# Performance work log

Measured on AMD Instinct MI355X. Metric: run time of the kernel, lower is better.

Reference implementation:

```python
import jax, jax.numpy as jnp
import numpy as np


def setup_inputs() -> dict:
    key = jax.random.key(0)
    kq, kk, kv = jax.random.split(key, 3)
    shape = (4, 8, 64, 8192)  # (b, n_heads, d, s)
    q = jax.random.normal(kq, shape, dtype=jnp.float32)
    k = jax.random.normal(kk, shape, dtype=jnp.float32)
    v = jax.random.normal(kv, shape, dtype=jnp.float32)
    return {"q": q, "k": k, "v": v}


def reference(q, k, v):
    # q, k, v: (b, n, d, s)
    q = jax.nn.softmax(q, axis=-2)        # softmax over feature dim d
    k = jax.nn.softmax(k, axis=-1)        # softmax over sequence dim s
    scale = q.shape[-2] ** (-0.5)
    q = q * scale
    # context: (b, n, d_k, d_v) = sum_s k[..., i, s] * v[..., j, s]
    context = jnp.einsum('bnis,bnjs->bnij', k, v)
    # out: (b, n, d_v, s)
    out = jnp.einsum('bnij,bnis->bnjs', context, q)
    return out
```

## Files before the change

kernel.cpp:

```cpp
#include <hip/hip_runtime.h>


typedef __attribute__((ext_vector_type(8))) short bf16x8;
typedef __attribute__((ext_vector_type(4))) float floatx4;

constexpr int D = 64, S = 8192, HEADS = 32;
constexpr int NC = 32;
constexpr int CHUNK = S / NC;

__device__ __forceinline__ short bf16_rn(float x) {
    unsigned u = __builtin_bit_cast(unsigned, x);
    return (short)((u + 0x8000u) >> 16);
}
__device__ __forceinline__ float bf16_f(short h) {
    unsigned u = ((unsigned)(unsigned short)h) << 16;
    return __builtin_bit_cast(float, u);
}
__device__ __forceinline__ void split8(const float* x, bf16x8& hi, bf16x8& lo) {
#pragma unroll
    for (int e = 0; e < 8; ++e) {
        short h = bf16_rn(x[e]);
        hi[e] = h;
        lo[e] = bf16_rn(x[e] - bf16_f(h));
    }
}

__global__ __launch_bounds__(256) void ctx_kernel(
    const float* __restrict__ K, const float* __restrict__ V,
    float* __restrict__ Cpart,
    float* __restrict__ Rpart)
{
    __shared__ float buf[16 * 4 * 64];
    __shared__ float rbuf[64];
    const int h = blockIdx.x, c = blockIdx.y;
    const int wave = threadIdx.x >> 6, lane = threadIdx.x & 63;
    const int m = lane & 15, quad = lane >> 4;

    const float* Kb = K + (size_t)h * D * S;
    const float* Vb = V + (size_t)h * D * S;

    floatx4 acc[4][4];
#pragma unroll
    for (int a = 0; a < 4; ++a)
#pragma unroll
        for (int b = 0; b < 4; ++b) acc[a][b] = (floatx4){0.f, 0.f, 0.f, 0.f};
    float rs[4] = {0.f, 0.f, 0.f, 0.f};

    float kraw[4][8], vraw[4][8];
    const int sw = c * CHUNK + wave * 64 + quad * 8;

#pragma unroll
    for (int mt = 0; mt < 4; ++mt) {
        const float* pk = Kb + (size_t)(mt * 16 + m) * S + sw;
        const float* pv = Vb + (size_t)(mt * 16 + m) * S + sw;
        *(float4*)&kraw[mt][0] = *(const float4*)pk;
        *(float4*)&kraw[mt][4] = *(const float4*)(pk + 4);
        *(float4*)&vraw[mt][0] = *(const float4*)pv;
        *(float4*)&vraw[mt][4] = *(const float4*)(pv + 4);
    }

    for (int it = 0; it < 2; ++it) {
        bf16x8 ah[4], al[4], bh[4], bl[4];
#pragma unroll
        for (int mt = 0; mt < 4; ++mt) {
            float ex[8];
#pragma unroll
            for (int e = 0; e < 8; ++e) {
                ex[e] = __expf(kraw[mt][e]);
                rs[mt] += ex[e];
            }
            split8(ex, ah[mt], al[mt]);
            split8(vraw[mt], bh[mt], bl[mt]);
        }
        if (it == 0) {
#pragma unroll
            for (int mt = 0; mt < 4; ++mt) {
                const float* pk = Kb + (size_t)(mt * 16 + m) * S + sw + 32;
                const float* pv = Vb + (size_t)(mt * 16 + m) * S + sw + 32;
                *(float4*)&kraw[mt][0] = *(const float4*)pk;
                *(float4*)&kraw[mt][4] = *(const float4*)(pk + 4);
                *(float4*)&vraw[mt][0] = *(const float4*)pv;
                *(float4*)&vraw[mt][4] = *(const float4*)(pv + 4);
            }
        }
#pragma unroll
        for (int mt = 0; mt < 4; ++mt)
#pragma unroll
            for (int nt = 0; nt < 4; ++nt) {
                acc[mt][nt] = __builtin_amdgcn_mfma_f32_16x16x32_bf16(
                    ah[mt], bh[nt], acc[mt][nt], 0, 0, 0);
                acc[mt][nt] = __builtin_amdgcn_mfma_f32_16x16x32_bf16(
                    ah[mt], bl[nt], acc[mt][nt], 0, 0, 0);
                acc[mt][nt] = __builtin_amdgcn_mfma_f32_16x16x32_bf16(
                    al[mt], bh[nt], acc[mt][nt], 0, 0, 0);
            }
    }

#pragma unroll
    for (int mt = 0; mt < 4; ++mt) {
        float v0 = rs[mt];
        v0 += __shfl_xor(v0, 16, 64);
        v0 += __shfl_xor(v0, 32, 64);
        rs[mt] = v0;
    }

    for (int w = 0; w < 4; ++w) {
        if (wave == w) {
#pragma unroll
            for (int mt = 0; mt < 4; ++mt) {
                if (lane < 16)
                    rbuf[mt * 16 + lane] =
                        (w == 0) ? rs[mt] : rbuf[mt * 16 + lane] + rs[mt];
#pragma unroll
                for (int nt = 0; nt < 4; ++nt)
#pragma unroll
                    for (int r = 0; r < 4; ++r) {
                        const int idx = ((mt * 4 + nt) * 4 + r) * 64 + lane;
                        buf[idx] = (w == 0) ? acc[mt][nt][r]
                                            : buf[idx] + acc[mt][nt][r];
                    }
            }
        }
        __syncthreads();
    }

    const size_t pbase = ((size_t)h * NC + c) * 4096;
    for (int idx = threadIdx.x; idx < 4096; idx += 256)
        Cpart[pbase + idx] = buf[idx];
    if (threadIdx.x < 64)
        Rpart[((size_t)h * NC + c) * 64 + threadIdx.x] = rbuf[threadIdx.x];
}

__global__ __launch_bounds__(256) void reduce_kernel(
    const float* __restrict__ Cpart, const float* __restrict__ Rpart,
    float* __restrict__ CnT)
{
    __shared__ float invr[D];
    const int h = blockIdx.x, t = threadIdx.x;

    if (t < D) {
        float s = 0.f;
#pragma unroll
        for (int c = 0; c < NC; ++c)
            s += Rpart[((size_t)h * NC + c) * 64 + t];
        invr[t] = 0.125f / s;
    }
    __syncthreads();

    for (int idx = t; idx < 4096; idx += 256) {
        float s = 0.f;
#pragma unroll
        for (int c = 0; c < NC; ++c)
            s += Cpart[((size_t)h * NC + c) * 4096 + idx];
        const int tile = idx >> 8, reg = (idx >> 6) & 3, lane = idx & 63;
        const int mt = tile >> 2, nt = tile & 3;
        const int i = mt * 16 + ((lane >> 4) << 2) + reg;
        const int j = nt * 16 + (lane & 15);
        CnT[(size_t)h * 4096 + j * 64 + i] = s * invr[i];
    }
}

__global__ __launch_bounds__(256) void out_kernel(
    const float* __restrict__ Q, const float* __restrict__ CnT,
    float* __restrict__ Out)
{
    const int h = blockIdx.x;
    const int wave = threadIdx.x >> 6, lane = threadIdx.x & 63;
    const int m = lane & 15, quad = lane >> 4;
    const int sbase = (blockIdx.y * 4 + wave) * 128;

    bf16x8 Ah[4][2], Al[4][2];
    const float* Cb = CnT + (size_t)h * 4096;
#pragma unroll
    for (int jt = 0; jt < 4; ++jt)
#pragma unroll
        for (int kk = 0; kk < 2; ++kk) {
            float a[8];
            const float* p = Cb + (jt * 16 + m) * 64 + kk * 32 + quad * 8;
            *(float4*)&a[0] = *(const float4*)p;
            *(float4*)&a[4] = *(const float4*)(p + 4);
            split8(a, Ah[jt][kk], Al[jt][kk]);
        }

    const float* Qb = Q + (size_t)h * D * S;
    float* Ob = Out + (size_t)h * D * S;

    for (int it = 0; it < 8; ++it) {
        const int scol = sbase + it * 16 + m;
        float e[16];
        float cs = 0.f;
#pragma unroll
        for (int kk = 0; kk < 2; ++kk)
#pragma unroll
            for (int j2 = 0; j2 < 8; ++j2) {
                const float qv = Qb[(size_t)(kk * 32 + quad * 8 + j2) * S + scol];
                const float ev = __expf(qv);
                e[kk * 8 + j2] = ev;
                cs += ev;
            }
        cs += __shfl_xor(cs, 16, 64);
        cs += __shfl_xor(cs, 32, 64);
        const float inv = 1.0f / cs;

        bf16x8 Bh[2], Bl[2];
        split8(&e[0], Bh[0], Bl[0]);
        split8(&e[8], Bh[1], Bl[1]);

#pragma unroll
        for (int jt = 0; jt < 4; ++jt) {
            floatx4 a = (floatx4){0.f, 0.f, 0.f, 0.f};
#pragma unroll
            for (int kk = 0; kk < 2; ++kk) {
                a = __builtin_amdgcn_mfma_f32_16x16x32_bf16(Ah[jt][kk], Bh[kk], a, 0, 0, 0);
                a = __builtin_amdgcn_mfma_f32_16x16x32_bf16(Ah[jt][kk], Bl[kk], a, 0, 0, 0);
                a = __builtin_amdgcn_mfma_f32_16x16x32_bf16(Al[jt][kk], Bh[kk], a, 0, 0, 0);
            }
#pragma unroll
            for (int r = 0; r < 4; ++r)
                Ob[(size_t)(jt * 16 + quad * 4 + r) * S + scol] = a[r] * inv;
        }
    }
}

extern "C" void kernel_launch(void* const* d_in, const int* in_sizes, int n_in,
                              void* d_out, int out_size, void* d_ws, size_t ws_size,
                              hipStream_t stream) {
    const float* q = (const float*)d_in[0];
    const float* k = (const float*)d_in[1];
    const float* v = (const float*)d_in[2];
    float* out = (float*)d_out;

    float* Cpart = (float*)d_ws;
    float* Rpart = Cpart + (size_t)HEADS * NC * 4096;
    float* CnT   = Rpart + (size_t)HEADS * NC * 64;

    ctx_kernel<<<dim3(HEADS, NC), 256, 0, stream>>>(k, v, Cpart, Rpart);
    reduce_kernel<<<dim3(HEADS), 256, 0, stream>>>(Cpart, Rpart, CnT);
    out_kernel<<<dim3(HEADS, 16), 256, 0, stream>>>(q, CnT, out);
}
```

Before: 265.8 us.

## Stream K/V tiles through double-buffered LDS via async global_load_lds in context kernel

The context kernel is restructured to use 512 threads per block. It stages 64-column K and V tiles into a swizzled, double-buffered LDS region with async global-to-LDS loads, and each wave owns a 16x32 slice of the 64x64 context, so the cross-wave LDS reduction is gone. The chunk count is halved, which means fewer partials to write and reduce, and the reduce kernel is spread across 8 blocks per head. The aim is to overlap memory traffic with exp/split/MFMA work and to cut partial-sum overhead. In exchange, exp and split work on V is redone by multiple waves, and the kernel now depends on hand-written waitcnt and barrier ordering.

```diff
diff --git a/kernel.cpp b/kernel.cpp
--- a/kernel.cpp
+++ b/kernel.cpp
@@ -1,12 +1,14 @@
 #include <hip/hip_runtime.h>
+#include <stdint.h>
 
 
 typedef __attribute__((ext_vector_type(8))) short bf16x8;
 typedef __attribute__((ext_vector_type(4))) float floatx4;
 
 constexpr int D = 64, S = 8192, HEADS = 32;
-constexpr int NC = 32;
+constexpr int NC = 16;
 constexpr int CHUNK = S / NC;
+constexpr int NT = CHUNK / 64;
 
 __device__ __forceinline__ short bf16_rn(float x) {
     unsigned u = __builtin_bit_cast(unsigned, x);
@@ -25,110 +27,107 @@
     }
 }
 
-__global__ __launch_bounds__(256) void ctx_kernel(
+__device__ __forceinline__ void gl16(const void* g, void* l) {
+    __builtin_amdgcn_global_load_lds(
+        (const __attribute__((address_space(1))) unsigned int*)g,
+        (__attribute__((address_space(3))) unsigned int*)l, 16, 0, 0);
+}
+
+__global__ __launch_bounds__(512, 4) void ctx_kernel(
     const float* __restrict__ K, const float* __restrict__ V,
     float* __restrict__ Cpart,
     float* __restrict__ Rpart)
 {
-    __shared__ float buf[16 * 4 * 64];
-    __shared__ float rbuf[64];
+    __shared__ char smem[2 * 2 * 16384];
     const int h = blockIdx.x, c = blockIdx.y;
     const int wave = threadIdx.x >> 6, lane = threadIdx.x & 63;
     const int m = lane & 15, quad = lane >> 4;
 
     const float* Kb = K + (size_t)h * D * S;
     const float* Vb = V + (size_t)h * D * S;
-
-    floatx4 acc[4][4];
-#pragma unroll
-    for (int a = 0; a < 4; ++a)
-#pragma unroll
-        for (int b = 0; b < 4; ++b) acc[a][b] = (floatx4){0.f, 0.f, 0.f, 0.f};
-    float rs[4] = {0.f, 0.f, 0.f, 0.f};
-
-    float kraw[4][8], vraw[4][8];
-    const int sw = c * CHUNK + wave * 64 + quad * 8;
-
-#pragma unroll
-    for (int mt = 0; mt < 4; ++mt) {
-        const float* pk = Kb + (size_t)(mt * 16 + m) * S + sw;
-        const float* pv = Vb + (size_t)(mt * 16 + m) * S + sw;
-        *(float4*)&kraw[mt][0] = *(const float4*)pk;
-        *(float4*)&kraw[mt][4] = *(const float4*)(pk + 4);
-        *(float4*)&vraw[mt][0] = *(const float4*)pv;
-        *(float4*)&vraw[mt][4] = *(const float4*)(pv + 4);
-    }
-
-    for (int it = 0; it < 2; ++it) {
-        bf16x8 ah[4], al[4], bh[4], bl[4];
-#pragma unroll
-        for (int mt = 0; mt < 4; ++mt) {
+    const int c0 = c * CHUNK;
+
+    const int ii = wave << 2;
+    const int smat = ii >> 4;
+    const int r0base = (ii & 15) << 2;
+    const float* gmat = smat ? Vb : Kb;
+
+    auto stage = [&](int buf, int t) {
+        const int colf = c0 + (t << 6);
+#pragma unroll
+        for (int g = 0; g < 4; ++g) {
+            const int r0 = r0base + (g << 2);
+            const int r = r0 + (lane >> 4);
+            const int su = (lane & 15) ^ (r & 7);
+            const float* src = gmat + (size_t)r * S + colf + (su << 2);
+            char* dst = smem + (buf << 15) + (smat << 14) + (r0 << 8);
+            gl16(src, dst);
+        }
+    };
+
+    const int mt = wave >> 1, nt0 = (wave & 1) << 1;
+    const int rA = mt * 16 + m;
+    floatx4 acc[2];
+    acc[0] = (floatx4){0.f, 0.f, 0.f, 0.f};
+    acc[1] = (floatx4){0.f, 0.f, 0.f, 0.f};
+    float rs = 0.f;
+
+    stage(0, 0);
+    for (int t = 0; t < NT; ++t) {
+        if (t + 1 < NT) {
+            stage((t + 1) & 1, t + 1);
+            asm volatile("s_waitcnt vmcnt(4)" ::: "memory");
+        } else {
+            asm volatile("s_waitcnt vmcnt(0)" ::: "memory");
+        }
+        asm volatile("s_barrier" ::: "memory");
+
+        const char* kb = smem + ((t & 1) << 15);
+        const char* vb = kb + 16384;
+#pragma unroll
+        for (int ks = 0; ks < 2; ++ks) {
+            const int u0 = (ks << 3) + (quad << 1);
+            float ar[8];
+            const char* kr = kb + (rA << 8);
+            *(float4*)&ar[0] = *(const float4*)(kr + ((u0 ^ (rA & 7)) << 4));
+            *(float4*)&ar[4] = *(const float4*)(kr + (((u0 + 1) ^ (rA & 7)) << 4));
             float ex[8];
 #pragma unroll
             for (int e = 0; e < 8; ++e) {
-                ex[e] = __expf(kraw[mt][e]);
-                rs[mt] += ex[e];
-            }
-            split8(ex, ah[mt], al[mt]);
-            split8(vraw[mt], bh[mt], bl[mt]);
-        }
-        if (it == 0) {
-#pragma unroll
-            for (int mt = 0; mt < 4; ++mt) {
-                const float* pk = Kb + (size_t)(mt * 16 + m) * S + sw + 32;
-                const float* pv = Vb + (size_t)(mt * 16 + m) * S + sw + 32;
-                *(float4*)&kraw[mt][0] = *(const float4*)pk;
-                *(float4*)&kraw[mt][4] = *(const float4*)(pk + 4);
-                *(float4*)&vraw[mt][0] = *(const float4*)pv;
-                *(float4*)&vraw[mt][4] = *(const float4*)(pv + 4);
-            }
-        }
-#pragma unroll
-        for (int mt = 0; mt < 4; ++mt)
-#pragma unroll
-            for (int nt = 0; nt < 4; ++nt) {
-                acc[mt][nt] = __builtin_amdgcn_mfma_f32_16x16x32_bf16(
-                    ah[mt], bh[nt], acc[mt][nt], 0, 0, 0);
-                acc[mt][nt] = __builtin_amdgcn_mfma_f32_16x16x32_bf16(
-                    ah[mt], bl[nt], acc[mt][nt], 0, 0, 0);
-                acc[mt][nt] = __builtin_amdgcn_mfma_f32_16x16x32_bf16(
-                    al[mt], bh[nt], acc[mt][nt], 0, 0, 0);
-            }
-    }
-
-#pragma unroll
-    for (int mt = 0; mt < 4; ++mt) {
-        float v0 = rs[mt];
-        v0 += __shfl_xor(v0, 16, 64);
-        v0 += __shfl_xor(v0, 32, 64);
-        rs[mt] = v0;
-    }
-
-    for (int w = 0; w < 4; ++w) {
-        if (wave == w) {
-#pragma unroll
-            for (int mt = 0; mt < 4; ++mt) {
-                if (lane < 16)
-                    rbuf[mt * 16 + lane] =
-                        (w == 0) ? rs[mt] : rbuf[mt * 16 + lane] + rs[mt];
-#pragma unroll
-                for (int nt = 0; nt < 4; ++nt)
-#pragma unroll
-                    for (int r = 0; r < 4; ++r) {
-                        const int idx = ((mt * 4 + nt) * 4 + r) * 64 + lane;
-                        buf[idx] = (w == 0) ? acc[mt][nt][r]
-                                            : buf[idx] + acc[mt][nt][r];
-                    }
-            }
-        }
-        __syncthreads();
-    }
-
-    const size_t pbase = ((size_t)h * NC + c) * 4096;
-    for (int idx = threadIdx.x; idx < 4096; idx += 256)
-        Cpart[pbase + idx] = buf[idx];
-    if (threadIdx.x < 64)
-        Rpart[((size_t)h * NC + c) * 64 + threadIdx.x] = rbuf[threadIdx.x];
+                ex[e] = __expf(ar[e]);
+                rs += ex[e];
+            }
+            bf16x8 ah, al;
+            split8(ex, ah, al);
+#pragma unroll
+            for (int j = 0; j < 2; ++j) {
+                const int rB = (nt0 + j) * 16 + m;
+                float br[8];
+                const char* vr = vb + (rB << 8);
+                *(float4*)&br[0] = *(const float4*)(vr + ((u0 ^ (rB & 7)) << 4));
+                *(float4*)&br[4] = *(const float4*)(vr + (((u0 + 1) ^ (rB & 7)) << 4));
+                bf16x8 bh, bl;
+                split8(br, bh, bl);
+                acc[j] = __builtin_amdgcn_mfma_f32_16x16x32_bf16(ah, bh, acc[j], 0, 0, 0);
+                acc[j] = __builtin_amdgcn_mfma_f32_16x16x32_bf16(ah, bl, acc[j], 0, 0, 0);
+                acc[j] = __builtin_amdgcn_mfma_f32_16x16x32_bf16(al, bh, acc[j], 0, 0, 0);
+            }
+        }
+        asm volatile("s_barrier" ::: "memory");
+    }
+
+    rs += __shfl_xor(rs, 16, 64);
+    rs += __shfl_xor(rs, 32, 64);
+
+    const size_t pbase = (((size_t)h * NC + c) << 12);
+#pragma unroll
+    for (int j = 0; j < 2; ++j)
+#pragma unroll
+        for (int r = 0; r < 4; ++r)
+            Cpart[pbase + ((size_t)(((mt * 4 + nt0 + j) * 4 + r)) << 6) + lane] =
+                acc[j][r];
+    if ((wave & 1) == 0 && lane < 16)
+        Rpart[(((size_t)h * NC + c) << 6) + mt * 16 + lane] = rs;
 }
 
 __global__ __launch_bounds__(256) void reduce_kernel(
@@ -136,27 +135,29 @@
     float* __restrict__ CnT)
 {
     __shared__ float invr[D];
-    const int h = blockIdx.x, t = threadIdx.x;
+    const int h = blockIdx.x, p = blockIdx.y, t = threadIdx.x;
 
     if (t < D) {
         float s = 0.f;
 #pragma unroll
         for (int c = 0; c < NC; ++c)
-            s += Rpart[((size_t)h * NC + c) * 64 + t];
+            s += Rpart[(((size_t)h * NC + c) << 6) + t];
         invr[t] = 0.125f / s;
     }
     __syncthreads();
 
-    for (int idx = t; idx < 4096; idx += 256) {
+#pragma unroll
+    for (int k = 0; k < 2; ++k) {
+        const int idx = (p << 9) + (k << 8) + t;
         float s = 0.f;
 #pragma unroll
         for (int c = 0; c < NC; ++c)
-            s += Cpart[((size_t)h * NC + c) * 4096 + idx];
+            s += Cpart[(((size_t)h * NC + c) << 12) + idx];
         const int tile = idx >> 8, reg = (idx >> 6) & 3, lane = idx & 63;
-        const int mt = tile >> 2, nt = tile & 3;
-        const int i = mt * 16 + ((lane >> 4) << 2) + reg;
-        const int j = nt * 16 + (lane & 15);
-        CnT[(size_t)h * 4096 + j * 64 + i] = s * invr[i];
+        const int mtl = tile >> 2, ntl = tile & 3;
+        const int i = mtl * 16 + ((lane >> 4) << 2) + reg;
+        const int j = ntl * 16 + (lane & 15);
+        CnT[((size_t)h << 12) + j * 64 + i] = s * invr[i];
     }
 }
 
@@ -234,7 +235,7 @@
     float* Rpart = Cpart + (size_t)HEADS * NC * 4096;
     float* CnT   = Rpart + (size_t)HEADS * NC * 64;
 
-    ctx_kernel<<<dim3(HEADS, NC), 256, 0, stream>>>(k, v, Cpart, Rpart);
-    reduce_kernel<<<dim3(HEADS), 256, 0, stream>>>(Cpart, Rpart, CnT);
+    ctx_kernel<<<dim3(HEADS, NC), 512, 0, stream>>>(k, v, Cpart, Rpart);
+    reduce_kernel<<<dim3(HEADS, 8), 256, 0, stream>>>(Cpart, Rpart, CnT);
     out_kernel<<<dim3(HEADS, 16), 256, 0, stream>>>(q, CnT, out);
 }
```

After: 253.3 us. 1.05x faster.
